# Performance work log

Hardware: AMD Instinct MI355X
Metric: run time of the kernel (lower is better)

## Reference

```python
import jax, jax.numpy as jnp
import numpy as np

EPS = 1e-5

def conv2d(x, w, b=None, pad=0, groups=1):
    # x: NCHW, w: OIHW
    y = jax.lax.conv_general_dilated(
        x, w, window_strides=(1, 1), padding=[(pad, pad), (pad, pad)],
        dimension_numbers=('NCHW', 'OIHW', 'NCHW'), feature_group_count=groups)
    if b is not None:
        y = y + b[None, :, None, None]
    return y

def layernorm_c(x, w, b):
    # WithBias LayerNorm over channel dim of NCHW (matches to_3d -> LN(last dim=c) -> to_4d)
    mu = jnp.mean(x, axis=1, keepdims=True)
    var = jnp.mean((x - mu) ** 2, axis=1, keepdims=True)
    return (x - mu) / jnp.sqrt(var + EPS) * w[None, :, None, None] + b[None, :, None, None]

def setup_inputs() -> dict:
    key = jax.random.key(0)
    ks = iter(jax.random.split(key, 40))
    C, C8, Cc, Cs = 64, 8, 21, 2  # dim, dim//8, dim//compress_ratio, dim//squeeze_factor
    H = W = 64
    B = 4
    Hm = 128  # mlp hidden = dim * mlp_ratio
    s = 0.05
    def rn(shape):
        return jax.random.normal(next(ks), shape, dtype=jnp.float32) * s
    return {
        'x': jax.random.normal(next(ks), (B, C, H, W), dtype=jnp.float32),
        'ln_w': jnp.ones((C,), jnp.float32),
        'ln_b': jnp.zeros((C,), jnp.float32),
        'sab_q_w': rn((C8, C, 1, 1)), 'sab_q_b': rn((C8,)),
        'sab_k_w': rn((C8, C, 1, 1)), 'sab_k_b': rn((C8,)),
        'sab_v_w': rn((C, C, 1, 1)), 'sab_v_b': rn((C,)),
        'sab_qkdw_w': rn((C8, 1, 3, 3)), 'sab_qkdw_b': rn((C8,)),
        'sab_vdw_w': rn((C, 1, 3, 3)), 'sab_vdw_b': rn((C,)),
        'sab_proj_w': rn((C, C, 1, 1)), 'sab_proj_b': rn((C,)),
        'sab_gamma': jnp.zeros((1,), jnp.float32) + 0.1,
        'cab_w1': rn((Cc, C, 3, 3)), 'cab_b1': rn((Cc,)),
        'cab_w2': rn((C, Cc, 3, 3)), 'cab_b2': rn((C,)),
        'ca_w1': rn((Cs, C, 1, 1)), 'ca_b1': rn((Cs,)),
        'ca_w2': rn((C, Cs, 1, 1)), 'ca_b2': rn((C,)),
        'fc1_w': rn((Hm, C)), 'fc1_b': rn((Hm,)),
        'fc2_w': rn((C, Hm)), 'fc2_b': rn((C,)),
    }

def reference(x, ln_w, ln_b,
              sab_q_w, sab_q_b, sab_k_w, sab_k_b, sab_v_w, sab_v_b,
              sab_qkdw_w, sab_qkdw_b, sab_vdw_w, sab_vdw_b,
              sab_proj_w, sab_proj_b, sab_gamma,
              cab_w1, cab_b1, cab_w2, cab_b2,
              ca_w1, ca_b1, ca_w2, ca_b2,
              fc1_w, fc1_b, fc2_w, fc2_b):
    b, c, h, w = x.shape
    hw = h * w
    shortcut = x
    xn = layernorm_c(x, ln_w, ln_b)

    # --- SAB: full-pixel spatial self-attention ---
    C8 = sab_q_w.shape[0]
    q = conv2d(conv2d(xn, sab_q_w, sab_q_b), sab_qkdw_w, sab_qkdw_b, pad=1, groups=C8)
    k = conv2d(conv2d(xn, sab_k_w, sab_k_b), sab_qkdw_w, sab_qkdw_b, pad=1, groups=C8)
    v = conv2d(conv2d(xn, sab_v_w, sab_v_b), sab_vdw_w, sab_vdw_b, pad=1, groups=c)
    qf = q.reshape(b, C8, hw)          # (b, c8, n)
    kf = k.reshape(b, C8, hw)
    vf = v.reshape(b, c, hw)
    energy = jnp.einsum('bdi,bdj->bij', qf, kf)      # (b, hw, hw)
    attn = jax.nn.softmax(energy, axis=-1)
    out = jnp.einsum('bcj,bij->bci', vf, attn)        # (b, c, hw)
    out = out.reshape(b, c, h, w)
    out = conv2d(out, sab_proj_w, sab_proj_b)
    sa_feat = sab_gamma[0] * out + xn

    # --- CAB: conv compress/expand + RCAN channel attention ---
    y = conv2d(xn, cab_w1, cab_b1, pad=1)
    y = jax.nn.gelu(y, approximate=False)
    y = conv2d(y, cab_w2, cab_b2, pad=1)
    p = jnp.mean(y, axis=(2, 3), keepdims=True)       # adaptive avg pool to 1x1
    p = jax.nn.relu(conv2d(p, ca_w1, ca_b1))
    p = jax.nn.sigmoid(conv2d(p, ca_w2, ca_b2))
    ca_feat = y * p

    feat_sum = sa_feat + ca_feat + shortcut

    # --- MLP over channels (note: output is reshaped, NOT permuted back — faithful to source) ---
    fs1 = layernorm_c(feat_sum, ln_w, ln_b)
    t = fs1.transpose(0, 2, 3, 1).reshape(b, hw, c)   # (b, hw, c)
    t = jax.nn.gelu(t @ fc1_w.T + fc1_b, approximate=False)
    t = t @ fc2_w.T + fc2_b
    feat_sum2 = t.reshape(b, c, h, w)                 # raw view, matching torch .view(b,c,h,w)
    return feat_sum2 + feat_sum
```

## Files before the change

kernel.cpp:

```cpp
#include <hip/hip_runtime.h>
#include <math.h>

#define NB 4
#define NC 64
#define NC8 8
#define NCC 21
#define NHW 4096
#define NHM 128

typedef __attribute__((ext_vector_type(8))) short bf16x8;
typedef __attribute__((ext_vector_type(8))) unsigned short ushort8;
typedef __attribute__((ext_vector_type(4))) float f32x4;

__device__ __forceinline__ float gelu_exact(float x) {
    return 0.5f * x * (1.0f + erff(x * 0.70710678118654752f));
}

__device__ __forceinline__ unsigned short f2bf(float x) {
    union { float f; unsigned u; } u; u.f = x;
    unsigned r = u.u + 0x7fffu + ((u.u >> 16) & 1u);
    return (unsigned short)(r >> 16);
}

__device__ __forceinline__ float bf2f(unsigned short v) {
    union { unsigned u; float f; } t; t.u = (unsigned)v << 16; return t.f;
}

__global__ __launch_bounds__(256) void k_prep(const float* __restrict__ qw, const float* __restrict__ kw,
                     const float* __restrict__ vw, const float* __restrict__ c1w,
                     const float* __restrict__ c2w, const float* __restrict__ pw,
                     const float* __restrict__ f1w, const float* __restrict__ f2w,
                     float* __restrict__ o, float* __restrict__ pool,
                     const float* __restrict__ x, const float* __restrict__ lnw,
                     const float* __restrict__ lnb,
                     unsigned short* __restrict__ xn, unsigned short* __restrict__ xnT) {
    int bid = blockIdx.x;
    int tid = threadIdx.x;
    if (bid < 244) {
        int idx = bid * 256 + tid;
        if (idx < 256) pool[idx] = 0.f;
        if (idx < 5120) {
            int ci = idx / 80, j = idx - ci * 80;
            float v = j < 8 ? qw[j * 64 + ci] : (j < 16 ? kw[(j - 8) * 64 + ci] : vw[(j - 16) * 64 + ci]);
            o[idx] = v;
        } else if (idx < 9216) {
            int r = idx - 5120; int co = r & 63, ci = r >> 6;
            o[idx] = pw[co * 64 + ci];
        } else if (idx < 17408) {
            int r = idx - 9216; int m = r & 127, c = r >> 7;
            o[idx] = f1w[m * 64 + c];
        } else if (idx < 25600) {
            int r = idx - 17408; int wo = r & 63, m = r >> 6;
            o[idx] = f2w[wo * 128 + m];
        } else if (idx < 44032) {
            int r = idx - 25600;
            int j = r & 7, l = (r >> 3) & 63, s = (r >> 9) % 18, f = r / 9216;
            int co = f * 16 + (l & 15);
            int k = s * 32 + (l >> 4) * 8 + j;
            int tap = k >> 6, ci = k & 63;
            float v = (co < 21) ? c1w[co * 576 + ci * 9 + tap] : 0.f;
            unsigned short hi = f2bf(v);
            unsigned short lo = f2bf(v - bf2f(hi));
            ((unsigned short*)(o + 25600))[r] = hi;
            ((unsigned short*)(o + 34816))[r] = lo;
        } else if (idx < 62464) {
            int r = idx - 44032;
            int j = r & 7, l = (r >> 3) & 63, s = (r >> 9) % 9, f = r / 4608;
            int co = f * 16 + (l & 15);
            int ci = (l >> 4) * 8 + j;
            float v = (ci < 21) ? c2w[co * 189 + ci * 9 + s] : 0.f;
            unsigned short hi = f2bf(v);
            unsigned short lo = f2bf(v - bf2f(hi));
            ((unsigned short*)(o + 44032))[r] = hi;
            ((unsigned short*)(o + 53248))[r] = lo;
        }
        return;
    }
    __shared__ float r1[4][64], r2[4][64];
    int lb = bid - 244;
    int pl = tid & 63, cq = tid >> 6;
    int b = lb >> 6;
    int pix = (lb & 63) * 64 + pl;
    const float* p = x + (size_t)b * NC * NHW + pix;
    float v[16]; float s = 0.f, ss = 0.f;
    #pragma unroll
    for (int k = 0; k < 16; ++k) {
        float f = p[(size_t)(cq * 16 + k) * NHW];
        v[k] = f; s += f; ss += f * f;
    }
    r1[cq][pl] = s; r2[cq][pl] = ss;
    __syncthreads();
    float S  = r1[0][pl] + r1[1][pl] + r1[2][pl] + r1[3][pl];
    float SS = r2[0][pl] + r2[1][pl] + r2[2][pl] + r2[3][pl];
    float mean = S * (1.0f / 64);
    float rstd = rsqrtf(SS * (1.0f / 64) - mean * mean + 1e-5f);
    unsigned short* q = xn + (size_t)b * NC * NHW + pix;
    ushort8 t0, t1;
    #pragma unroll
    for (int k = 0; k < 16; ++k) {
        int c = cq * 16 + k;
        unsigned short bv = f2bf((v[k] - mean) * rstd * lnw[c] + lnb[c]);
        q[(size_t)c * NHW] = bv;
        if (k < 8) t0[k] = bv; else t1[k - 8] = bv;
    }
    unsigned short* tp = xnT + ((size_t)b * NHW + pix) * 64 + cq * 16;
    *(ushort8*)tp = t0;
    *(ushort8*)(tp + 8) = t1;
}

__global__ __launch_bounds__(512) void k_qkv(const unsigned short* __restrict__ xn,
        const float* __restrict__ wt, const float* __restrict__ qb,
        const float* __restrict__ kb, const float* __restrict__ vb,
        unsigned short* __restrict__ q1, unsigned short* __restrict__ k1,
        unsigned short* __restrict__ v1) {
    __shared__ unsigned short Xs[64][64];
    __shared__ float Ws[64][80];
    int tid = threadIdx.x;
    int pix0 = blockIdx.x * 64, b = blockIdx.y;
    for (int i = tid; i < 1024; i += 512) {
        int c = i >> 4, q4 = i & 15;
        *(ushort4*)&Xs[c][q4 * 4] = *(const ushort4*)(xn + ((size_t)b * NC + c) * NHW + pix0 + q4 * 4);
    }
    for (int i = tid; i < 1280; i += 512)
        *(float4*)&((float*)Ws)[i * 4] = *(const float4*)&wt[i * 4];
    __syncthreads();
    int p2 = (tid & 31) * 2, g = tid >> 5;
    int co0 = g * 5;
    float a0[5], a1[5];
    #pragma unroll
    for (int j = 0; j < 5; ++j) { a0[j] = 0.f; a1[j] = 0.f; }
    for (int ci = 0; ci < 64; ++ci) {
        ushort2 uv = *(const ushort2*)&Xs[ci][p2];
        float fx = bf2f(uv.x), fy = bf2f(uv.y);
        #pragma unroll
        for (int j = 0; j < 5; ++j) {
            float wv = Ws[ci][co0 + j];
            a0[j] = fmaf(fx, wv, a0[j]);
            a1[j] = fmaf(fy, wv, a1[j]);
        }
    }
    #pragma unroll
    for (int j = 0; j < 5; ++j) {
        int co = co0 + j;
        float bsv; unsigned short* dst;
        if (co < 8)       { bsv = qb[co];      dst = q1 + ((size_t)b * NC8 + co) * NHW + pix0 + p2; }
        else if (co < 16) { bsv = kb[co - 8];  dst = k1 + ((size_t)b * NC8 + co - 8) * NHW + pix0 + p2; }
        else              { bsv = vb[co - 16]; dst = v1 + ((size_t)b * NC + co - 16) * NHW + pix0 + p2; }
        ushort2 o = { f2bf(a0[j] + bsv), f2bf(a1[j] + bsv) };
        *(ushort2*)dst = o;
    }
}

__global__ __launch_bounds__(512) void k_dwcab1(
        const unsigned short* __restrict__ q1, const unsigned short* __restrict__ k1,
        const unsigned short* __restrict__ v1,
        const float* __restrict__ qkw, const float* __restrict__ qkb,
        const float* __restrict__ vw, const float* __restrict__ vb,
        unsigned short* __restrict__ qdb, unsigned short* __restrict__ kdb,
        unsigned short* __restrict__ v8,
        const unsigned short* __restrict__ xnT,
        const unsigned short* __restrict__ Ah, const unsigned short* __restrict__ Al,
        const float* __restrict__ bias, unsigned short* __restrict__ y1T) {
    __shared__ float Rs[2048];
    int bid = blockIdx.x;
    int tid = threadIdx.x;
    if (bid < 2560) {
        int pix = (bid & 7) * 512 + tid;
        int rest = bid >> 3;
        int yv = rest % 80, b = rest / 80;
        int y = pix >> 6, x = pix & 63;
        if (yv < 16) {
            int c = yv & 7;
            const unsigned short* ip = (yv < 8 ? q1 : k1) + ((size_t)b * NC8 + c) * NHW;
            const float* wp = qkw + c * 9;
            float acc = qkb[c];
            #pragma unroll
            for (int dy = -1; dy <= 1; ++dy) {
                int yy = y + dy; if (yy < 0 || yy > 63) continue;
                #pragma unroll
                for (int dx = -1; dx <= 1; ++dx) {
                    int xx = x + dx; if (xx < 0 || xx > 63) continue;
                    acc += wp[(dy + 1) * 3 + (dx + 1)] * bf2f(ip[yy * 64 + xx]);
                }
            }
            (yv < 8 ? qdb : kdb)[((size_t)b * NHW + pix) * NC8 + c] = f2bf(acc);
        } else {
            int c = yv - 16;
            const unsigned short* ip = v1 + ((size_t)b * NC + c) * NHW;
            const float* wp = vw + c * 9;
            float acc = vb[c];
            #pragma unroll
            for (int dy = -1; dy <= 1; ++dy) {
                int yy = y + dy; if (yy < 0 || yy > 63) continue;
                #pragma unroll
                for (int dx = -1; dx <= 1; ++dx) {
                    int xx = x + dx; if (xx < 0 || xx > 63) continue;
                    acc += wp[(dy + 1) * 3 + (dx + 1)] * bf2f(ip[yy * 64 + xx]);
                }
            }
            v8[(((size_t)b * 512 + (pix >> 3)) * NC + c) * 8 + (pix & 7)] = f2bf(acc);
        }
        return;
    }
    int r = bid - 2560;
    int y = r & 63, b = r >> 6;
    int w = tid >> 6, lane = tid & 63;
    int il = lane & 15, g = lane >> 4;
    int frag = w & 3, kh = w >> 2;
    int xloc = frag * 16 + il;
    f32x4 acc[2];
    acc[0] = (f32x4){0.f, 0.f, 0.f, 0.f};
    acc[1] = (f32x4){0.f, 0.f, 0.f, 0.f};
    #pragma unroll
    for (int si = 0; si < 9; ++si) {
        int s = kh * 9 + si;
        int tap = s >> 1;
        int ci0 = (s & 1) * 32;
        int dyv = tap / 3 - 1, dxv = tap - (tap / 3) * 3 - 1;
        int xx = xloc + dxv, yy = y + dyv;
        bf16x8 bv = (bf16x8)(short)0;
        if (((unsigned)xx < 64u) && ((unsigned)yy < 64u))
            bv = *(const bf16x8*)(xnT + ((size_t)b * NHW + yy * 64 + xx) * 64 + ci0 + g * 8);
        #pragma unroll
        for (int f = 0; f < 2; ++f) {
            bf16x8 ahv = *(const bf16x8*)(Ah + ((size_t)(f * 18 + s) * 64 + lane) * 8);
            bf16x8 alv = *(const bf16x8*)(Al + ((size_t)(f * 18 + s) * 64 + lane) * 8);
            acc[f] = __builtin_amdgcn_mfma_f32_16x16x32_bf16(ahv, bv, acc[f], 0, 0, 0);
            acc[f] = __builtin_amdgcn_mfma_f32_16x16x32_bf16(alv, bv, acc[f], 0, 0, 0);
        }
    }
    if (kh == 1) {
        #pragma unroll
        for (int f = 0; f < 2; ++f)
            #pragma unroll
            for (int e = 0; e < 4; ++e)
                Rs[((frag * 2 + f) * 4 + e) * 64 + lane] = acc[f][e];
    }
    __syncthreads();
    if (kh == 0) {
        #pragma unroll
        for (int f = 0; f < 2; ++f) {
            ushort4 pk;
            #pragma unroll
            for (int e = 0; e < 4; ++e) {
                float v = acc[f][e] + Rs[((frag * 2 + f) * 4 + e) * 64 + lane];
                int co = f * 16 + g * 4 + e;
                float rr = 0.f;
                if (co < 21) rr = gelu_exact(v + bias[co]);
                ((unsigned short*)&pk)[e] = f2bf(rr);
            }
            *(ushort4*)(y1T + ((size_t)b * NHW + y * 64 + xloc) * 32 + f * 16 + g * 4) = pk;
        }
    }
}

__global__ __launch_bounds__(512) void k_flashcab2(
        const unsigned short* __restrict__ qdb, const unsigned short* __restrict__ kdb,
        const unsigned short* __restrict__ v8, unsigned short* __restrict__ O,
        const unsigned short* __restrict__ y1T,
        const unsigned short* __restrict__ Ah, const unsigned short* __restrict__ Al,
        const float* __restrict__ bias, unsigned short* __restrict__ ycT,
        float* __restrict__ pool) {
    __shared__ __align__(16) char smem[35840];
    int bid = blockIdx.x;
    int tid = threadIdx.x;
    int w = tid >> 6, lane = tid & 63;
    int g = lane >> 4, il = lane & 15;
    if (bid < 512) {
        int i0 = (bid & 127) * 32, b = bid >> 7;
        unsigned short (*P)[72] = (unsigned short (*)[72])(smem + w * 2304);
        bf16x8 qb0 = (bf16x8)(short)0, qb1 = (bf16x8)(short)0;
        if (g == 0) {
            qb0 = *(const bf16x8*)(qdb + (size_t)(b * NHW + i0 + il) * NC8);
            qb1 = *(const bf16x8*)(qdb + (size_t)(b * NHW + i0 + 16 + il) * NC8);
        }
        f32x4 acc0[4], acc1[4];
        #pragma unroll
        for (int ct = 0; ct < 4; ++ct) {
            acc0[ct] = (f32x4){0.f, 0.f, 0.f, 0.f};
            acc1[ct] = (f32x4){0.f, 0.f, 0.f, 0.f};
        }
        float La0 = 0.f, La1 = 0.f;
        bf16x8 kn[4];
        #pragma unroll
        for (int t = 0; t < 4; ++t) {
            kn[t] = (bf16x8)(short)0;
            if (g == 0) kn[t] = *(const bf16x8*)(kdb + (size_t)(b * NHW + w * 512 + 16 * t + il) * NC8);
        }
        for (int jt = 0; jt < 8; ++jt) {
            int j0 = w * 512 + jt * 64;
            int ch0 = b * 512 + (j0 >> 3);
            bf16x8 va[2][4];
            #pragma unroll
            for (int kc = 0; kc < 2; ++kc)
                #pragma unroll
                for (int ct = 0; ct < 4; ++ct)
                    va[kc][ct] = *(const bf16x8*)(v8 +
                        ((size_t)(ch0 + kc * 4 + g) * NC + ct * 16 + il) * 8);
            bf16x8 ka[4];
            #pragma unroll
            for (int t = 0; t < 4; ++t) ka[t] = kn[t];
            if (jt < 7) {
                #pragma unroll
                for (int t = 0; t < 4; ++t) {
                    kn[t] = (bf16x8)(short)0;
                    if (g == 0) kn[t] = *(const bf16x8*)(kdb + (size_t)(b * NHW + j0 + 64 + 16 * t + il) * NC8);
                }
            }
            #pragma unroll
            for (int t = 0; t < 4; ++t) {
                f32x4 sv = __builtin_amdgcn_mfma_f32_16x16x32_bf16(ka[t], qb0, (f32x4){0.f, 0.f, 0.f, 0.f}, 0, 0, 0);
                float p0 = __expf(sv[0]), p1 = __expf(sv[1]);
                float p2 = __expf(sv[2]), p3 = __expf(sv[3]);
                La0 += (p0 + p1) + (p2 + p3);
                ushort4 pk;
                pk.x = f2bf(p0); pk.y = f2bf(p1); pk.z = f2bf(p2); pk.w = f2bf(p3);
                *(ushort4*)&P[il][16 * t + 4 * g] = pk;
            }
            #pragma unroll
            for (int kc = 0; kc < 2; ++kc) {
                bf16x8 pb = *(const bf16x8*)&P[il][kc * 32 + 8 * g];
                #pragma unroll
                for (int ct = 0; ct < 4; ++ct)
                    acc0[ct] = __builtin_amdgcn_mfma_f32_16x16x32_bf16(va[kc][ct], pb, acc0[ct], 0, 0, 0);
            }
            #pragma unroll
            for (int t = 0; t < 4; ++t) {
                f32x4 sv = __builtin_amdgcn_mfma_f32_16x16x32_bf16(ka[t], qb1, (f32x4){0.f, 0.f, 0.f, 0.f}, 0, 0, 0);
                float p0 = __expf(sv[0]), p1 = __expf(sv[1]);
                float p2 = __expf(sv[2]), p3 = __expf(sv[3]);
                La1 += (p0 + p1) + (p2 + p3);
                ushort4 pk;
                pk.x = f2bf(p0); pk.y = f2bf(p1); pk.z = f2bf(p2); pk.w = f2bf(p3);
                *(ushort4*)&P[il][16 * t + 4 * g] = pk;
            }
            #pragma unroll
            for (int kc = 0; kc < 2; ++kc) {
                bf16x8 pb = *(const bf16x8*)&P[il][kc * 32 + 8 * g];
                #pragma unroll
                for (int ct = 0; ct < 4; ++ct)
                    acc1[ct] = __builtin_amdgcn_mfma_f32_16x16x32_bf16(va[kc][ct], pb, acc1[ct], 0, 0, 0);
            }
        }
        La0 += __shfl_xor(La0, 16, 64); La0 += __shfl_xor(La0, 32, 64);
        La1 += __shfl_xor(La1, 16, 64); La1 += __shfl_xor(La1, 32, 64);

        __syncthreads();
        unsigned short* Ocm = (unsigned short*)smem;
        float* Lw = (float*)(smem + 34816);
        #pragma unroll
        for (int ct = 0; ct < 4; ++ct)
            #pragma unroll
            for (int e = 0; e < 4; ++e) {
                int c = ct * 16 + 4 * g + e;
                Ocm[(w * 2 + 0) * 1088 + c * 17 + il] = f2bf(acc0[ct][e]);
                Ocm[(w * 2 + 1) * 1088 + c * 17 + il] = f2bf(acc1[ct][e]);
            }
        if (lane < 16) {
            Lw[(w * 2 + 0) * 16 + il] = La0;
            Lw[(w * 2 + 1) * 16 + il] = La1;
        }
        __syncthreads();

        int st = tid >> 8, rem = tid & 255;
        int ic = rem & 15, ch = rem >> 4;
        float l = 0.f;
        #pragma unroll
        for (int w2 = 0; w2 < 8; ++w2) l += Lw[(w2 * 2 + st) * 16 + ic];
        float rl = 1.0f / l;
        #pragma unroll
        for (int cc = 0; cc < 4; ++cc) {
            int c = cc * 16 + ch;
            float o = 0.f;
            #pragma unroll
            for (int w2 = 0; w2 < 8; ++w2) o += bf2f(Ocm[(w2 * 2 + st) * 1088 + c * 17 + ic]);
            O[(size_t)(b * NC + c) * NHW + i0 + st * 16 + ic] = f2bf(o * rl);
        }
        return;
    }
    float* Rs = (float*)smem;
    float (*Ssum)[64] = (float (*)[64])(smem + 16384);
    int r = bid - 512;
    int y = r & 63, b = r >> 6;
    int frag = w & 3, kh = w >> 2;
    int xloc = frag * 16 + il;
    f32x4 acc[4];
    #pragma unroll
    for (int f = 0; f < 4; ++f) acc[f] = (f32x4){0.f, 0.f, 0.f, 0.f};
    #pragma unroll
    for (int si = 0; si < 5; ++si) {
        if (!(kh == 1 && si == 4)) {
            int s = kh * 5 + si;
            int dyv = s / 3 - 1, dxv = s - (s / 3) * 3 - 1;
            int xx = xloc + dxv, yy = y + dyv;
            bf16x8 bv = (bf16x8)(short)0;
            if (((unsigned)xx < 64u) && ((unsigned)yy < 64u))
                bv = *(const bf16x8*)(y1T + ((size_t)b * NHW + yy * 64 + xx) * 32 + g * 8);
            #pragma unroll
            for (int f = 0; f < 4; ++f) {
                bf16x8 ahv = *(const bf16x8*)(Ah + ((size_t)(f * 9 + s) * 64 + lane) * 8);
                bf16x8 alv = *(const bf16x8*)(Al + ((size_t)(f * 9 + s) * 64 + lane) * 8);
                acc[f] = __builtin_amdgcn_mfma_f32_16x16x32_bf16(ahv, bv, acc[f], 0, 0, 0);
                acc[f] = __builtin_amdgcn_mfma_f32_16x16x32_bf16(alv, bv, acc[f], 0, 0, 0);
            }
        }
    }
    if (kh == 1) {
        #pragma unroll
        for (int f = 0; f < 4; ++f)
            #pragma unroll
            for (int e = 0; e < 4; ++e)
                Rs[((frag * 4 + f) * 4 + e) * 64 + lane] = acc[f][e];
    }
    __syncthreads();
    if (kh == 0) {
        #pragma unroll
        for (int f = 0; f < 4; ++f) {
            ushort4 pk;
            #pragma unroll
            for (int e = 0; e < 4; ++e) {
                int co = f * 16 + g * 4 + e;
                float v = acc[f][e] + Rs[((frag * 4 + f) * 4 + e) * 64 + lane] + bias[co];
                ((unsigned short*)&pk)[e] = f2bf(v);
                float ps = v;
                ps += __shfl_xor(ps, 1, 64);
                ps += __shfl_xor(ps, 2, 64);
                ps += __shfl_xor(ps, 4, 64);
                ps += __shfl_xor(ps, 8, 64);
                if (il == 0) Ssum[frag][co] = ps;
            }
            *(ushort4*)(ycT + ((size_t)b * NHW + y * 64 + xloc) * 64 + f * 16 + g * 4) = pk;
        }
    }
    __syncthreads();
    if (tid < 64) {
        float t = Ssum[0][tid] + Ssum[1][tid] + Ssum[2][tid] + Ssum[3][tid];
        atomicAdd(&pool[b * NC + tid], t);
    }
}

__global__ __launch_bounds__(512) void k_fsum2(const unsigned short* __restrict__ O,
        const float* __restrict__ pwt, const float* __restrict__ pb,
        const float* __restrict__ gamma, const unsigned short* __restrict__ xnT,
        const unsigned short* __restrict__ ycT, const float* __restrict__ pool,
        const float* __restrict__ cw1, const float* __restrict__ cb1,
        const float* __restrict__ cw2, const float* __restrict__ cb2,
        const float* __restrict__ x, const float* __restrict__ lnw,
        const float* __restrict__ lnb, unsigned short* __restrict__ fsum,
        unsigned short* __restrict__ fs1) {
    __shared__ unsigned short Os[64][64];
    __shared__ float Ws[64][64];
    __shared__ float Fs[64][66];
    __shared__ float mean_s[64], rstd_s[64];
    int tid = threadIdx.x;
    int pix0 = blockIdx.x * 64, b = blockIdx.y;
    for (int i = tid; i < 1024; i += 512) {
        int c = i >> 4, q4 = i & 15;
        *(ushort4*)&Os[c][q4 * 4] = *(const ushort4*)(O + ((size_t)b * NC + c) * NHW + pix0 + q4 * 4);
    }
    for (int i = tid; i < 1024; i += 512)
        *(float4*)&((float*)Ws)[i * 4] = *(const float4*)&pwt[i * 4];
    __syncthreads();
    float h0 = cb1[0], h1 = cb1[1];
    for (int ci = 0; ci < NC; ++ci) {
        float pv = pool[b * NC + ci] * (1.0f / NHW);
        h0 += cw1[ci] * pv;
        h1 += cw1[NC + ci] * pv;
    }
    h0 = fmaxf(h0, 0.f); h1 = fmaxf(h1, 0.f);
    int p2 = (tid & 31) * 2, g = tid >> 5;
    int co0 = g * 4;
    float scv[4];
    #pragma unroll
    for (int j = 0; j < 4; ++j) {
        int c = co0 + j;
        float z = cw2[c * 2] * h0 + cw2[c * 2 + 1] * h1 + cb2[c];
        scv[j] = 1.0f / (1.0f + __expf(-z));
    }
    float a0[4], a1[4];
    #pragma unroll
    for (int j = 0; j < 4; ++j) { a0[j] = 0.f; a1[j] = 0.f; }
    for (int ci = 0; ci < 64; ++ci) {
        ushort2 uv = *(const ushort2*)&Os[ci][p2];
        float ox = bf2f(uv.x), oy = bf2f(uv.y);
        float wv[4];
        *(float4*)wv = *(const float4*)&Ws[ci][co0];
        #pragma unroll
        for (int j = 0; j < 4; ++j) {
            a0[j] = fmaf(ox, wv[j], a0[j]);
            a1[j] = fmaf(oy, wv[j], a1[j]);
        }
    }
    float gg = gamma[0];
    size_t base = (size_t)b * NC * NHW + pix0 + p2;
    const unsigned short* xtp = xnT + ((size_t)b * NHW + pix0 + p2) * 64 + co0;
    const unsigned short* ytp = ycT + ((size_t)b * NHW + pix0 + p2) * 64 + co0;
    ushort4 xa = *(const ushort4*)xtp, xb = *(const ushort4*)(xtp + 64);
    ushort4 ya = *(const ushort4*)ytp, yb = *(const ushort4*)(ytp + 64);
    float f0[4], f1[4];
    #pragma unroll
    for (int j = 0; j < 4; ++j) {
        int c = co0 + j;
        size_t n = base + (size_t)c * NHW;
        float pbv = pb[c];
        float2 xv = *(const float2*)&x[n];
        f0[j] = gg * (a0[j] + pbv) + bf2f(((const unsigned short*)&xa)[j])
              + bf2f(((const unsigned short*)&ya)[j]) * scv[j] + xv.x;
        f1[j] = gg * (a1[j] + pbv) + bf2f(((const unsigned short*)&xb)[j])
              + bf2f(((const unsigned short*)&yb)[j]) * scv[j] + xv.y;
        ushort2 o = { f2bf(f0[j]), f2bf(f1[j]) };
        *(ushort2*)&fsum[n] = o;
        Fs[c][p2] = f0[j]; Fs[c][p2 + 1] = f1[j];
    }
    __syncthreads();
    if (tid < 64) {
        float s = 0.f, ss = 0.f;
        for (int c = 0; c < 64; ++c) { float v = Fs[c][tid]; s += v; ss += v * v; }
        float mean = s * (1.0f / 64);
        mean_s[tid] = mean;
        rstd_s[tid] = rsqrtf(ss * (1.0f / 64) - mean * mean + 1e-5f);
    }
    __syncthreads();
    float m0 = mean_s[p2], r0 = rstd_s[p2];
    float m1 = mean_s[p2 + 1], r1 = rstd_s[p2 + 1];
    #pragma unroll
    for (int j = 0; j < 4; ++j) {
        int c = co0 + j;
        size_t n = base + (size_t)c * NHW;
        float lw = lnw[c], lb = lnb[c];
        ushort2 o = { f2bf((f0[j] - m0) * r0 * lw + lb),
                      f2bf((f1[j] - m1) * r1 * lw + lb) };
        *(ushort2*)&fs1[n] = o;
    }
}

__global__ __launch_bounds__(512) void k_mlp(const unsigned short* __restrict__ fs1,
        const float* __restrict__ w1t, const float* __restrict__ b1,
        const float* __restrict__ w2t, const float* __restrict__ b2,
        const unsigned short* __restrict__ fs, float* __restrict__ out) {
    __shared__ unsigned short Fs[64][64];
    __shared__ float W1[64][128];
    __shared__ unsigned short Hs[128][64];
    __shared__ float W2[128][64];
    int tid = threadIdx.x;
    int pix0 = blockIdx.x * 64, b = blockIdx.y;
    for (int i = tid; i < 1024; i += 512) {
        int c = i >> 4, q4 = i & 15;
        *(ushort4*)&Fs[c][q4 * 4] = *(const ushort4*)(fs1 + ((size_t)b * NC + c) * NHW + pix0 + q4 * 4);
    }
    for (int i = tid; i < 2048; i += 512)
        *(float4*)&((float*)W1)[i * 4] = *(const float4*)&w1t[i * 4];
    for (int i = tid; i < 2048; i += 512)
        *(float4*)&((float*)W2)[i * 4] = *(const float4*)&w2t[i * 4];
    __syncthreads();
    int p2 = (tid & 31) * 2, g = tid >> 5;
    {
        int m0 = g * 8;
        float a0[8], a1[8];
        #pragma unroll
        for (int j = 0; j < 8; ++j) { float bv = b1[m0 + j]; a0[j] = bv; a1[j] = bv; }
        for (int c = 0; c < 64; ++c) {
            ushort2 uv = *(const ushort2*)&Fs[c][p2];
            float vx = bf2f(uv.x), vy = bf2f(uv.y);
            float wv[8];
            *(float4*)&wv[0] = *(const float4*)&W1[c][m0];
            *(float4*)&wv[4] = *(const float4*)&W1[c][m0 + 4];
            #pragma unroll
            for (int j = 0; j < 8; ++j) {
                a0[j] = fmaf(vx, wv[j], a0[j]);
                a1[j] = fmaf(vy, wv[j], a1[j]);
            }
        }
        #pragma unroll
        for (int j = 0; j < 8; ++j) {
            ushort2 o = { f2bf(gelu_exact(a0[j])), f2bf(gelu_exact(a1[j])) };
            *(ushort2*)&Hs[m0 + j][p2] = o;
        }
    }
    __syncthreads();
    int wo0 = g * 4;
    float a0[4], a1[4];
    #pragma unroll
    for (int j = 0; j < 4; ++j) { float bv = b2[wo0 + j]; a0[j] = bv; a1[j] = bv; }
    for (int m = 0; m < 128; ++m) {
        ushort2 uv = *(const ushort2*)&Hs[m][p2];
        float vx = bf2f(uv.x), vy = bf2f(uv.y);
        float wv[4];
        *(float4*)wv = *(const float4*)&W2[m][wo0];
        #pragma unroll
        for (int j = 0; j < 4; ++j) {
            a0[j] = fmaf(vx, wv[j], a0[j]);
            a1[j] = fmaf(vy, wv[j], a1[j]);
        }
    }
    size_t ob0 = ((size_t)b * NHW + pix0 + p2) * 64 + wo0;
    ushort4 r0 = *(const ushort4*)&fs[ob0];
    ushort4 r1 = *(const ushort4*)&fs[ob0 + 64];
    float4 w0, w1;
    w0.x = a0[0] + bf2f(r0.x); w0.y = a0[1] + bf2f(r0.y);
    w0.z = a0[2] + bf2f(r0.z); w0.w = a0[3] + bf2f(r0.w);
    w1.x = a1[0] + bf2f(r1.x); w1.y = a1[1] + bf2f(r1.y);
    w1.z = a1[2] + bf2f(r1.z); w1.w = a1[3] + bf2f(r1.w);
    *(float4*)&out[ob0] = w0;
    *(float4*)&out[ob0 + 64] = w1;
}

extern "C" void kernel_launch(void* const* d_in, const int* in_sizes, int n_in,
                              void* d_out, int out_size, void* d_ws, size_t ws_size,
                              hipStream_t stream) {
    const float* x        = (const float*)d_in[0];
    const float* ln_w     = (const float*)d_in[1];
    const float* ln_b     = (const float*)d_in[2];
    const float* q_w      = (const float*)d_in[3];
    const float* q_b      = (const float*)d_in[4];
    const float* k_w      = (const float*)d_in[5];
    const float* k_b      = (const float*)d_in[6];
    const float* v_w      = (const float*)d_in[7];
    const float* v_b      = (const float*)d_in[8];
    const float* qkdw_w   = (const float*)d_in[9];
    const float* qkdw_b   = (const float*)d_in[10];
    const float* vdw_w    = (const float*)d_in[11];
    const float* vdw_b    = (const float*)d_in[12];
    const float* proj_w   = (const float*)d_in[13];
    const float* proj_b   = (const float*)d_in[14];
    const float* gamma    = (const float*)d_in[15];
    const float* cab_w1   = (const float*)d_in[16];
    const float* cab_b1   = (const float*)d_in[17];
    const float* cab_w2   = (const float*)d_in[18];
    const float* cab_b2   = (const float*)d_in[19];
    const float* ca_w1    = (const float*)d_in[20];
    const float* ca_b1    = (const float*)d_in[21];
    const float* ca_w2    = (const float*)d_in[22];
    const float* ca_b2    = (const float*)d_in[23];
    const float* fc1_w    = (const float*)d_in[24];
    const float* fc1_b    = (const float*)d_in[25];
    const float* fc2_w    = (const float*)d_in[26];
    const float* fc2_b    = (const float*)d_in[27];
    float* out = (float*)d_out;

    char* ws = (char*)d_ws;
    size_t off = 0;
    auto alloc = [&](size_t bytes) { void* p = ws + off; off += (bytes + 255) & ~(size_t)255; return p; };
    unsigned short* xn  = (unsigned short*)alloc((size_t)NB * NC * NHW * 2);
    unsigned short* xnT = (unsigned short*)alloc((size_t)NB * NHW * NC * 2);
    unsigned short* q1  = (unsigned short*)alloc((size_t)NB * NC8 * NHW * 2);
    unsigned short* k1  = (unsigned short*)alloc((size_t)NB * NC8 * NHW * 2);
    unsigned short* v1  = (unsigned short*)alloc((size_t)NB * NC * NHW * 2);
    unsigned short* qdb = (unsigned short*)alloc((size_t)NB * NHW * NC8 * 2);
    unsigned short* kdb = (unsigned short*)alloc((size_t)NB * NHW * NC8 * 2);
    unsigned short* vdb = (unsigned short*)alloc((size_t)NB * NC * NHW * 2);
    unsigned short* O   = (unsigned short*)alloc((size_t)NB * NC * NHW * 2);
    unsigned short* y1T = (unsigned short*)alloc((size_t)NB * NHW * 32 * 2);
    unsigned short* ycT = (unsigned short*)alloc((size_t)NB * NHW * NC * 2);
    float* pool  = (float*)alloc(256 * 4);
    unsigned short* fsum = (unsigned short*)alloc((size_t)NB * NC * NHW * 2);
    unsigned short* fs1  = (unsigned short*)alloc((size_t)NB * NC * NHW * 2);
    float* wpack = (float*)alloc(62464 * 4);

    float* qkv_wt  = wpack;
    float* proj_wt = wpack + 5120;
    float* fc1_wt  = wpack + 9216;
    float* fc2_wt  = wpack + 17408;
    unsigned short* cab1Ah = (unsigned short*)(wpack + 25600);
    unsigned short* cab1Al = (unsigned short*)(wpack + 34816);
    unsigned short* cab2Ah = (unsigned short*)(wpack + 44032);
    unsigned short* cab2Al = (unsigned short*)(wpack + 53248);

    dim3 blk(256);
    dim3 blk5(512);

    k_prep<<<dim3(500), blk, 0, stream>>>(q_w, k_w, v_w, cab_w1, cab_w2, proj_w, fc1_w, fc2_w,
                                          wpack, pool, x, ln_w, ln_b, xn, xnT);
    k_qkv<<<dim3(64, NB), blk5, 0, stream>>>(xn, qkv_wt, q_b, k_b, v_b, q1, k1, v1);
    k_dwcab1<<<dim3(2816), blk5, 0, stream>>>(q1, k1, v1, qkdw_w, qkdw_b, vdw_w, vdw_b,
                                              qdb, kdb, vdb, xnT, cab1Ah, cab1Al, cab_b1, y1T);
    k_flashcab2<<<dim3(768), blk5, 0, stream>>>(qdb, kdb, vdb, O, y1T, cab2Ah, cab2Al,
                                                cab_b2, ycT, pool);
    k_fsum2<<<dim3(64, NB), blk5, 0, stream>>>(O, proj_wt, proj_b, gamma, xnT, ycT, pool,
                                               ca_w1, ca_b1, ca_w2, ca_b2, x, ln_w, ln_b,
                                               fsum, fs1);
    k_mlp<<<dim3(64, NB), blk5, 0, stream>>>(fs1, fc1_wt, fc1_b, fc2_wt, fc2_b, fsum, out);
}
```

Baseline: 201.8 us.

## Run MLP fc1/fc2 on bf16 MFMA with hi/lo split weights and transposed input

The MLP kernel switches from scalar FP32 FMAs over shared-memory weights to bf16 MFMA 16x16x32 instructions. Weights are pre-split into hi/lo bf16 fragments in the prep kernel to keep near-FP32 weight accuracy. The layernormed activation is now written pixel-major (fs1T) so each lane can load it directly as an MFMA B operand. This removes large shared-memory weight staging and scalar FMA work in k_mlp, at the cost of bf16 activation precision and twice the MFMA issues.

```diff
diff --git a/kernel.cpp b/kernel.cpp
--- a/kernel.cpp
+++ b/kernel.cpp
@@ -46,14 +46,8 @@
         } else if (idx < 9216) {
             int r = idx - 5120; int co = r & 63, ci = r >> 6;
             o[idx] = pw[co * 64 + ci];
-        } else if (idx < 17408) {
-            int r = idx - 9216; int m = r & 127, c = r >> 7;
-            o[idx] = f1w[m * 64 + c];
-        } else if (idx < 25600) {
-            int r = idx - 17408; int wo = r & 63, m = r >> 6;
-            o[idx] = f2w[wo * 128 + m];
-        } else if (idx < 44032) {
-            int r = idx - 25600;
+        } else if (idx < 27648) {
+            int r = idx - 9216;
             int j = r & 7, l = (r >> 3) & 63, s = (r >> 9) % 18, f = r / 9216;
             int co = f * 16 + (l & 15);
             int k = s * 32 + (l >> 4) * 8 + j;
@@ -61,18 +55,40 @@
             float v = (co < 21) ? c1w[co * 576 + ci * 9 + tap] : 0.f;
             unsigned short hi = f2bf(v);
             unsigned short lo = f2bf(v - bf2f(hi));
-            ((unsigned short*)(o + 25600))[r] = hi;
-            ((unsigned short*)(o + 34816))[r] = lo;
-        } else if (idx < 62464) {
-            int r = idx - 44032;
+            ((unsigned short*)(o + 9216))[r] = hi;
+            ((unsigned short*)(o + 18432))[r] = lo;
+        } else if (idx < 46080) {
+            int r = idx - 27648;
             int j = r & 7, l = (r >> 3) & 63, s = (r >> 9) % 9, f = r / 4608;
             int co = f * 16 + (l & 15);
             int ci = (l >> 4) * 8 + j;
             float v = (ci < 21) ? c2w[co * 189 + ci * 9 + s] : 0.f;
             unsigned short hi = f2bf(v);
             unsigned short lo = f2bf(v - bf2f(hi));
-            ((unsigned short*)(o + 44032))[r] = hi;
-            ((unsigned short*)(o + 53248))[r] = lo;
+            ((unsigned short*)(o + 27648))[r] = hi;
+            ((unsigned short*)(o + 36864))[r] = lo;
+        } else if (idx < 54272) {
+            int r = idx - 46080;
+            int j = r & 7, l = (r >> 3) & 63, q = r >> 9;
+            int F = q >> 1, s = q & 1;
+            int m = F * 16 + (l & 15);
+            int k = s * 32 + (l >> 4) * 8 + j;
+            float v = f1w[m * 64 + k];
+            unsigned short hi = f2bf(v);
+            unsigned short lo = f2bf(v - bf2f(hi));
+            ((unsigned short*)(o + 46080))[r] = hi;
+            ((unsigned short*)(o + 50176))[r] = lo;
+        } else if (idx < 62464) {
+            int r = idx - 54272;
+            int j = r & 7, l = (r >> 3) & 63, q = r >> 9;
+            int F2 = q >> 2, s = q & 3;
+            int wo = F2 * 16 + (l & 15);
+            int k = s * 32 + (l >> 4) * 8 + j;
+            float v = f2w[wo * 128 + k];
+            unsigned short hi = f2bf(v);
+            unsigned short lo = f2bf(v - bf2f(hi));
+            ((unsigned short*)(o + 54272))[r] = hi;
+            ((unsigned short*)(o + 58368))[r] = lo;
         }
         return;
     }
@@ -447,7 +463,7 @@
         const float* __restrict__ cw2, const float* __restrict__ cb2,
         const float* __restrict__ x, const float* __restrict__ lnw,
         const float* __restrict__ lnb, unsigned short* __restrict__ fsum,
-        unsigned short* __restrict__ fs1) {
+        unsigned short* __restrict__ fs1T) {
     __shared__ unsigned short Os[64][64];
     __shared__ float Ws[64][64];
     __shared__ float Fs[64][66];
@@ -523,86 +539,88 @@
     __syncthreads();
     float m0 = mean_s[p2], r0 = rstd_s[p2];
     float m1 = mean_s[p2 + 1], r1 = rstd_s[p2 + 1];
+    ushort4 oA, oB;
     #pragma unroll
     for (int j = 0; j < 4; ++j) {
         int c = co0 + j;
-        size_t n = base + (size_t)c * NHW;
         float lw = lnw[c], lb = lnb[c];
-        ushort2 o = { f2bf((f0[j] - m0) * r0 * lw + lb),
-                      f2bf((f1[j] - m1) * r1 * lw + lb) };
-        *(ushort2*)&fs1[n] = o;
-    }
-}
-
-__global__ __launch_bounds__(512) void k_mlp(const unsigned short* __restrict__ fs1,
-        const float* __restrict__ w1t, const float* __restrict__ b1,
-        const float* __restrict__ w2t, const float* __restrict__ b2,
+        ((unsigned short*)&oA)[j] = f2bf((f0[j] - m0) * r0 * lw + lb);
+        ((unsigned short*)&oB)[j] = f2bf((f1[j] - m1) * r1 * lw + lb);
+    }
+    unsigned short* fp = fs1T + ((size_t)b * NHW + pix0 + p2) * 64 + co0;
+    *(ushort4*)fp = oA;
+    *(ushort4*)(fp + 64) = oB;
+}
+
+__global__ __launch_bounds__(512) void k_mlp(const unsigned short* __restrict__ fs1T,
+        const unsigned short* __restrict__ A1h, const unsigned short* __restrict__ A1l,
+        const float* __restrict__ b1,
+        const unsigned short* __restrict__ A2h, const unsigned short* __restrict__ A2l,
+        const float* __restrict__ b2,
         const unsigned short* __restrict__ fs, float* __restrict__ out) {
-    __shared__ unsigned short Fs[64][64];
-    __shared__ float W1[64][128];
-    __shared__ unsigned short Hs[128][64];
-    __shared__ float W2[128][64];
+    __shared__ unsigned short Hs[64][136];
     int tid = threadIdx.x;
-    int pix0 = blockIdx.x * 64, b = blockIdx.y;
-    for (int i = tid; i < 1024; i += 512) {
-        int c = i >> 4, q4 = i & 15;
-        *(ushort4*)&Fs[c][q4 * 4] = *(const ushort4*)(fs1 + ((size_t)b * NC + c) * NHW + pix0 + q4 * 4);
-    }
-    for (int i = tid; i < 2048; i += 512)
-        *(float4*)&((float*)W1)[i * 4] = *(const float4*)&w1t[i * 4];
-    for (int i = tid; i < 2048; i += 512)
-        *(float4*)&((float*)W2)[i * 4] = *(const float4*)&w2t[i * 4];
-    __syncthreads();
-    int p2 = (tid & 31) * 2, g = tid >> 5;
-    {
-        int m0 = g * 8;
-        float a0[8], a1[8];
-        #pragma unroll
-        for (int j = 0; j < 8; ++j) { float bv = b1[m0 + j]; a0[j] = bv; a1[j] = bv; }
-        for (int c = 0; c < 64; ++c) {
-            ushort2 uv = *(const ushort2*)&Fs[c][p2];
-            float vx = bf2f(uv.x), vy = bf2f(uv.y);
-            float wv[8];
-            *(float4*)&wv[0] = *(const float4*)&W1[c][m0];
-            *(float4*)&wv[4] = *(const float4*)&W1[c][m0 + 4];
-            #pragma unroll
-            for (int j = 0; j < 8; ++j) {
-                a0[j] = fmaf(vx, wv[j], a0[j]);
-                a1[j] = fmaf(vy, wv[j], a1[j]);
-            }
-        }
-        #pragma unroll
-        for (int j = 0; j < 8; ++j) {
-            ushort2 o = { f2bf(gelu_exact(a0[j])), f2bf(gelu_exact(a1[j])) };
-            *(ushort2*)&Hs[m0 + j][p2] = o;
-        }
-    }
-    __syncthreads();
-    int wo0 = g * 4;
-    float a0[4], a1[4];
-    #pragma unroll
-    for (int j = 0; j < 4; ++j) { float bv = b2[wo0 + j]; a0[j] = bv; a1[j] = bv; }
-    for (int m = 0; m < 128; ++m) {
-        ushort2 uv = *(const ushort2*)&Hs[m][p2];
-        float vx = bf2f(uv.x), vy = bf2f(uv.y);
-        float wv[4];
-        *(float4*)wv = *(const float4*)&W2[m][wo0];
-        #pragma unroll
-        for (int j = 0; j < 4; ++j) {
-            a0[j] = fmaf(vx, wv[j], a0[j]);
-            a1[j] = fmaf(vy, wv[j], a1[j]);
-        }
-    }
-    size_t ob0 = ((size_t)b * NHW + pix0 + p2) * 64 + wo0;
-    ushort4 r0 = *(const ushort4*)&fs[ob0];
-    ushort4 r1 = *(const ushort4*)&fs[ob0 + 64];
-    float4 w0, w1;
-    w0.x = a0[0] + bf2f(r0.x); w0.y = a0[1] + bf2f(r0.y);
-    w0.z = a0[2] + bf2f(r0.z); w0.w = a0[3] + bf2f(r0.w);
-    w1.x = a1[0] + bf2f(r1.x); w1.y = a1[1] + bf2f(r1.y);
-    w1.z = a1[2] + bf2f(r1.z); w1.w = a1[3] + bf2f(r1.w);
-    *(float4*)&out[ob0] = w0;
-    *(float4*)&out[ob0 + 64] = w1;
+    int w = tid >> 6, lane = tid & 63;
+    int il = lane & 15, g = lane >> 4;
+    int frag = w & 3, fh = w >> 2;
+    int y = blockIdx.x, b = blockIdx.y;
+    int xloc = frag * 16 + il;
+    const unsigned short* bp = fs1T + ((size_t)b * NHW + y * 64 + xloc) * 64;
+    f32x4 acc[4];
+    #pragma unroll
+    for (int fi = 0; fi < 4; ++fi) acc[fi] = (f32x4){0.f, 0.f, 0.f, 0.f};
+    #pragma unroll
+    for (int s = 0; s < 2; ++s) {
+        bf16x8 bv = *(const bf16x8*)(bp + s * 32 + g * 8);
+        #pragma unroll
+        for (int fi = 0; fi < 4; ++fi) {
+            int F = fh * 4 + fi;
+            bf16x8 ah = *(const bf16x8*)(A1h + ((size_t)(F * 2 + s) * 64 + lane) * 8);
+            bf16x8 al = *(const bf16x8*)(A1l + ((size_t)(F * 2 + s) * 64 + lane) * 8);
+            acc[fi] = __builtin_amdgcn_mfma_f32_16x16x32_bf16(ah, bv, acc[fi], 0, 0, 0);
+            acc[fi] = __builtin_amdgcn_mfma_f32_16x16x32_bf16(al, bv, acc[fi], 0, 0, 0);
+        }
+    }
+    #pragma unroll
+    for (int fi = 0; fi < 4; ++fi) {
+        int F = fh * 4 + fi;
+        ushort4 pk;
+        #pragma unroll
+        for (int e = 0; e < 4; ++e) {
+            int m = F * 16 + g * 4 + e;
+            ((unsigned short*)&pk)[e] = f2bf(gelu_exact(acc[fi][e] + b1[m]));
+        }
+        *(ushort4*)&Hs[xloc][F * 16 + g * 4] = pk;
+    }
+    __syncthreads();
+    f32x4 acc2[2];
+    acc2[0] = (f32x4){0.f, 0.f, 0.f, 0.f};
+    acc2[1] = (f32x4){0.f, 0.f, 0.f, 0.f};
+    #pragma unroll
+    for (int s = 0; s < 4; ++s) {
+        bf16x8 bv = *(const bf16x8*)&Hs[xloc][s * 32 + g * 8];
+        #pragma unroll
+        for (int fi = 0; fi < 2; ++fi) {
+            int F2 = fh * 2 + fi;
+            bf16x8 ah = *(const bf16x8*)(A2h + ((size_t)(F2 * 4 + s) * 64 + lane) * 8);
+            bf16x8 al = *(const bf16x8*)(A2l + ((size_t)(F2 * 4 + s) * 64 + lane) * 8);
+            acc2[fi] = __builtin_amdgcn_mfma_f32_16x16x32_bf16(ah, bv, acc2[fi], 0, 0, 0);
+            acc2[fi] = __builtin_amdgcn_mfma_f32_16x16x32_bf16(al, bv, acc2[fi], 0, 0, 0);
+        }
+    }
+    #pragma unroll
+    for (int fi = 0; fi < 2; ++fi) {
+        int F2 = fh * 2 + fi;
+        int c0 = F2 * 16 + g * 4;
+        size_t ob = ((size_t)b * NHW + y * 64 + xloc) * 64 + c0;
+        ushort4 rv = *(const ushort4*)&fs[ob];
+        float4 o4;
+        o4.x = acc2[fi][0] + b2[c0 + 0] + bf2f(rv.x);
+        o4.y = acc2[fi][1] + b2[c0 + 1] + bf2f(rv.y);
+        o4.z = acc2[fi][2] + b2[c0 + 2] + bf2f(rv.z);
+        o4.w = acc2[fi][3] + b2[c0 + 3] + bf2f(rv.w);
+        *(float4*)&out[ob] = o4;
+    }
 }
 
 extern "C" void kernel_launch(void* const* d_in, const int* in_sizes, int n_in,
@@ -654,17 +672,19 @@
     unsigned short* ycT = (unsigned short*)alloc((size_t)NB * NHW * NC * 2);
     float* pool  = (float*)alloc(256 * 4);
     unsigned short* fsum = (unsigned short*)alloc((size_t)NB * NC * NHW * 2);
-    unsigned short* fs1  = (unsigned short*)alloc((size_t)NB * NC * NHW * 2);
+    unsigned short* fs1T = (unsigned short*)alloc((size_t)NB * NHW * NC * 2);
     float* wpack = (float*)alloc(62464 * 4);
 
     float* qkv_wt  = wpack;
     float* proj_wt = wpack + 5120;
-    float* fc1_wt  = wpack + 9216;
-    float* fc2_wt  = wpack + 17408;
-    unsigned short* cab1Ah = (unsigned short*)(wpack + 25600);
-    unsigned short* cab1Al = (unsigned short*)(wpack + 34816);
-    unsigned short* cab2Ah = (unsigned short*)(wpack + 44032);
-    unsigned short* cab2Al = (unsigned short*)(wpack + 53248);
+    unsigned short* cab1Ah = (unsigned short*)(wpack + 9216);
+    unsigned short* cab1Al = (unsigned short*)(wpack + 18432);
+    unsigned short* cab2Ah = (unsigned short*)(wpack + 27648);
+    unsigned short* cab2Al = (unsigned short*)(wpack + 36864);
+    unsigned short* fc1h   = (unsigned short*)(wpack + 46080);
+    unsigned short* fc1l   = (unsigned short*)(wpack + 50176);
+    unsigned short* fc2h   = (unsigned short*)(wpack + 54272);
+    unsigned short* fc2l   = (unsigned short*)(wpack + 58368);
 
     dim3 blk(256);
     dim3 blk5(512);
@@ -678,6 +698,7 @@
                                                 cab_b2, ycT, pool);
     k_fsum2<<<dim3(64, NB), blk5, 0, stream>>>(O, proj_wt, proj_b, gamma, xnT, ycT, pool,
                                                ca_w1, ca_b1, ca_w2, ca_b2, x, ln_w, ln_b,
-                                               fsum, fs1);
-    k_mlp<<<dim3(64, NB), blk5, 0, stream>>>(fs1, fc1_wt, fc1_b, fc2_wt, fc2_b, fsum, out);
-}
+                                               fsum, fs1T);
+    k_mlp<<<dim3(64, NB), blk5, 0, stream>>>(fs1T, fc1h, fc1l, fc1_b, fc2h, fc2l, fc2_b,
+                                             fsum, out);
+}
```

New measurement: 190.7 us. 5.5% less time.
